# Kernel tuning notes

Measured on AMD Instinct MI355X. Metric: run time of the kernel, lower is better.

Reference implementation:

```python
import jax, jax.numpy as jnp
import numpy as np

B, S, E = 2, 2048, 2048
H, D = 16, 128
I = 8192
EPS = 1e-5


def layernorm(x, w, b):
    mu = jnp.mean(x, axis=-1, keepdims=True)
    var = jnp.mean(jnp.square(x - mu), axis=-1, keepdims=True)
    return (x - mu) * jax.lax.rsqrt(var + EPS) * w + b


def setup_inputs() -> dict:
    key = jax.random.key(0)
    ks = jax.random.split(key, 6)
    s = 0.02
    return {
        "x": jax.random.normal(ks[0], (B, S, E), jnp.float32),
        "ln1_w": jnp.ones((E,), jnp.float32),
        "ln1_b": jnp.zeros((E,), jnp.float32),
        "Wqkv": jax.random.normal(ks[1], (E, 3 * E), jnp.float32) * s,
        "Wo": jax.random.normal(ks[2], (E, E), jnp.float32) * s,
        "ln2_w": jnp.ones((E,), jnp.float32),
        "ln2_b": jnp.zeros((E,), jnp.float32),
        "W1": jax.random.normal(ks[3], (E, I), jnp.float32) * s,
        "W2": jax.random.normal(ks[4], (I, E), jnp.float32) * s,
    }


def reference(x, ln1_w, ln1_b, Wqkv, Wo, ln2_w, ln2_b, W1, W2):
    scale = D ** -0.5
    # --- attention sublayer (pre-LN) ---
    h = layernorm(x, ln1_w, ln1_b)
    qkv = (h @ Wqkv).reshape(B, S, 3, H, D)
    q, k, v = [jnp.moveaxis(qkv[:, :, i], 1, 2) for i in range(3)]  # [B,H,S,D]
    scores = jnp.einsum("bhqd,bhkd->bhqk", q, k) * scale
    causal = jnp.triu(jnp.ones((S, S), bool), k=1)
    scores = jnp.where(causal, -jnp.inf, scores)
    attn = jax.nn.softmax(scores, axis=-1)
    out = jnp.einsum("bhqk,bhkd->bqhd", attn, v).reshape(B, S, E)
    x = x + out @ Wo
    # --- FFN sublayer (pre-LN) ---
    h = layernorm(x, ln2_w, ln2_b)
    x = x + jax.nn.gelu(h @ W1, approximate=True) @ W2
    return x
```

## Files before the change

kernel.cpp:

```cpp
#include <hip/hip_runtime.h>
#include <hip/hip_bf16.h>

#define B_ 2
#define S_ 2048
#define E_ 2048
#define H_ 16
#define D_ 128
#define I_ 8192
#define T_ (B_*S_)

typedef __attribute__((ext_vector_type(8))) short bf16x8;
typedef __attribute__((ext_vector_type(8))) unsigned short us8;
typedef __attribute__((ext_vector_type(4))) float f32x4;

__device__ __forceinline__ unsigned short f2bf(float f) {
  union { float f; unsigned int u; } c; c.f = f;
  unsigned int u = c.u;
  unsigned int r = (u + 0x7fffu + ((u >> 16) & 1u)) >> 16;
  return (unsigned short)r;
}

__device__ __forceinline__ void gload16(const void* g, void* l) {
  __builtin_amdgcn_global_load_lds((const __attribute__((address_space(1))) void*)g,
                                   (__attribute__((address_space(3))) void*)l, 16, 0, 0);
}

__global__ void transpose_w(const float* __restrict__ in, unsigned short* __restrict__ out,
                            int K, int N) {
  __shared__ float tile[32][33];
  const int n0 = blockIdx.x * 32, k0 = blockIdx.y * 32;
  const int tx = threadIdx.x, ty = threadIdx.y;
#pragma unroll
  for (int j = 0; j < 4; ++j) {
    int k = k0 + ty + j * 8;
    tile[ty + j * 8][tx] = in[(size_t)k * N + n0 + tx];
  }
  __syncthreads();
#pragma unroll
  for (int j = 0; j < 4; ++j) {
    int n = n0 + ty + j * 8;
    out[(size_t)n * K + k0 + tx] = f2bf(tile[tx][ty + j * 8]);
  }
}

__global__ void ln_kernel(const float* __restrict__ x, const float* __restrict__ w,
                          const float* __restrict__ b, unsigned short* __restrict__ out) {
  const int row = blockIdx.x;
  const int tid = threadIdx.x;
  const int wid = tid >> 6, lane = tid & 63;
  const float4* xr = (const float4*)(x + (size_t)row * E_);
  float4 v0 = xr[tid * 2], v1 = xr[tid * 2 + 1];
  float s  = v0.x + v0.y + v0.z + v0.w + v1.x + v1.y + v1.z + v1.w;
  float sq = v0.x*v0.x + v0.y*v0.y + v0.z*v0.z + v0.w*v0.w
           + v1.x*v1.x + v1.y*v1.y + v1.z*v1.z + v1.w*v1.w;
#pragma unroll
  for (int off = 32; off > 0; off >>= 1) {
    s  += __shfl_xor(s, off);
    sq += __shfl_xor(sq, off);
  }
  __shared__ float red[8];
  if (lane == 0) { red[wid] = s; red[wid + 4] = sq; }
  __syncthreads();
  s  = red[0] + red[1] + red[2] + red[3];
  sq = red[4] + red[5] + red[6] + red[7];
  const float mu  = s * (1.0f / E_);
  const float var = sq * (1.0f / E_) - mu * mu;
  const float rstd = rsqrtf(var + 1e-5f);
  const float4* w4 = (const float4*)w + tid * 2;
  const float4* b4 = (const float4*)b + tid * 2;
  float4 w0 = w4[0], w1 = w4[1], bb0 = b4[0], bb1 = b4[1];
  us8 o;
  o[0] = f2bf((v0.x - mu) * rstd * w0.x + bb0.x);
  o[1] = f2bf((v0.y - mu) * rstd * w0.y + bb0.y);
  o[2] = f2bf((v0.z - mu) * rstd * w0.z + bb0.z);
  o[3] = f2bf((v0.w - mu) * rstd * w0.w + bb0.w);
  o[4] = f2bf((v1.x - mu) * rstd * w1.x + bb1.x);
  o[5] = f2bf((v1.y - mu) * rstd * w1.y + bb1.y);
  o[6] = f2bf((v1.z - mu) * rstd * w1.z + bb1.z);
  o[7] = f2bf((v1.w - mu) * rstd * w1.w + bb1.w);
  *(us8*)(&out[(size_t)row * E_ + tid * 8]) = o;
}

template<int EPI>
__global__ void gemm_bt(const unsigned short* __restrict__ A,
                        const unsigned short* __restrict__ Bt,
                        void* __restrict__ Cout,
                        const float* __restrict__ resid,
                        int M, int N, int K) {
  __shared__ __align__(16) unsigned short As[128 * 32];
  __shared__ __align__(16) unsigned short Bs[128 * 32];
  const int gn = N >> 7;
  const int nwg = (M >> 7) * gn;
  const int cpx = nwg >> 3;
  const int bid = blockIdx.x;
  const int swz = (bid & 7) * cpx + (bid >> 3);
  const int bm = swz / gn, bn = swz % gn;
  const int tid = threadIdx.x;
  const int wid = tid >> 6, lane = tid & 63;
  const int fr = lane & 15, kg = lane >> 4;
  const int wr = wid >> 1, wc = wid & 1;

  const int c0 = wid * 2;
  const unsigned short* gA = A  + (size_t)(bm * 128 + c0 * 16 + (lane >> 2)) * K + (lane & 3) * 8;
  const unsigned short* gB = Bt + (size_t)(bn * 128 + c0 * 16 + (lane >> 2)) * K + (lane & 3) * 8;
  unsigned short* lA = &As[c0 * 512];
  unsigned short* lB = &Bs[c0 * 512];

  const unsigned short* rA = &As[(wr * 64 + fr) * 32 + kg * 8];
  const unsigned short* rB = &Bs[(wc * 64 + fr) * 32 + kg * 8];

  f32x4 acc[4][4] = {};
  const int nk = K >> 5;
  for (int kt = 0; kt < nk; ++kt) {
    __syncthreads();
    gload16(gA,                 lA);
    gload16(gA + 16 * (size_t)K, lA + 512);
    gload16(gB,                 lB);
    gload16(gB + 16 * (size_t)K, lB + 512);
    gA += 32; gB += 32;
    __syncthreads();
    bf16x8 af[4], bfr[4];
#pragma unroll
    for (int m = 0; m < 4; ++m) af[m]  = *(const bf16x8*)(rA + m * 16 * 32);
#pragma unroll
    for (int n = 0; n < 4; ++n) bfr[n] = *(const bf16x8*)(rB + n * 16 * 32);
#pragma unroll
    for (int m = 0; m < 4; ++m)
#pragma unroll
      for (int n = 0; n < 4; ++n)
        acc[m][n] = __builtin_amdgcn_mfma_f32_16x16x32_bf16(af[m], bfr[n], acc[m][n], 0, 0, 0);
  }

  const int row0 = bm * 128 + wr * 64;
  const int col0 = bn * 128 + wc * 64;
#pragma unroll
  for (int m = 0; m < 4; ++m) {
#pragma unroll
    for (int n = 0; n < 4; ++n) {
#pragma unroll
      for (int r = 0; r < 4; ++r) {
        const int row = row0 + m * 16 + kg * 4 + r;
        const int col = col0 + n * 16 + fr;
        const size_t idx = (size_t)row * N + col;
        const float v = acc[m][n][r];
        if constexpr (EPI == 0) {
          ((unsigned short*)Cout)[idx] = f2bf(v);
        } else if constexpr (EPI == 1) {
          const float u = 0.7978845608028654f * (v + 0.044715f * v * v * v);
          const float gel = 0.5f * v * (1.0f + tanhf(u));
          ((unsigned short*)Cout)[idx] = f2bf(gel);
        } else {
          ((float*)Cout)[idx] = v + resid[idx];
        }
      }
    }
  }
}

__global__ void extract_vT(const unsigned short* __restrict__ qkv, unsigned short* __restrict__ vT) {
  __shared__ unsigned short tile[32][34];
  const int bh = blockIdx.z;
  const int b = bh >> 4, h = bh & 15;
  const int s0 = blockIdx.y * 32, d0 = blockIdx.x * 32;
  const int tx = threadIdx.x, ty = threadIdx.y;
#pragma unroll
  for (int j = 0; j < 4; ++j) {
    int s = s0 + ty + j * 8;
    tile[ty + j * 8][tx] = qkv[(size_t)(b * S_ + s) * 6144 + 4096 + h * 128 + d0 + tx];
  }
  __syncthreads();
#pragma unroll
  for (int j = 0; j < 4; ++j) {
    int d = d0 + ty + j * 8;
    vT[((size_t)bh * 128 + d) * 2048 + s0 + tx] = tile[tx][ty + j * 8];
  }
}

__global__ void attn_kernel(const unsigned short* __restrict__ qkv,
                            const unsigned short* __restrict__ vT,
                            unsigned short* __restrict__ outp) {
  __shared__ __align__(16) unsigned short Ks[64 * 136];
  __shared__ __align__(16) unsigned short Vts[128 * 72];
  __shared__ __align__(16) unsigned short Ps[4 * 16 * 40];
  const int qt = blockIdx.x;
  const int bh = blockIdx.y;
  const int b = bh >> 4, h = bh & 15;
  const int tid = threadIdx.x, wid = tid >> 6, lane = tid & 63;
  const int fr = lane & 15, g = lane >> 4;

  const unsigned short* qptr = qkv + (size_t)(b * S_ + qt * 64 + wid * 16 + fr) * 6144 + h * 128;
  bf16x8 qf[4];
#pragma unroll
  for (int dc = 0; dc < 4; ++dc) qf[dc] = *(const bf16x8*)(qptr + dc * 32 + g * 8);

  float m0[4], l0[4];
#pragma unroll
  for (int r = 0; r < 4; ++r) { m0[r] = -1e30f; l0[r] = 0.0f; }
  f32x4 acc[8] = {};

  const unsigned short* kbase = qkv + (size_t)(b * S_) * 6144 + 2048 + h * 128;
  const unsigned short* vbase = vT + (size_t)bh * 128 * 2048;
  unsigned short* Pw = &Ps[wid * 640];
  const float scale = 0.08838834764831845f;

  for (int kt = 0; kt <= qt; ++kt) {
#pragma unroll
    for (int j = 0; j < 4; ++j) {
      int cc = tid + 256 * j;
      int krow = cc >> 4, cp = cc & 15;
      us8 v = *(const us8*)(kbase + (size_t)(kt * 64 + krow) * 6144 + cp * 8);
      *(us8*)(&Ks[krow * 136 + cp * 8]) = v;
    }
#pragma unroll
    for (int j = 0; j < 4; ++j) {
      int cc = tid + 256 * j;
      int drow = cc >> 3, cp = cc & 7;
      us8 v = *(const us8*)(vbase + (size_t)drow * 2048 + kt * 64 + cp * 8);
      *(us8*)(&Vts[drow * 72 + cp * 8]) = v;
    }
    __syncthreads();
    const bool diag = (kt == qt);
    for (int half = 0; half < 2; ++half) {
      f32x4 sc[2] = {};
#pragma unroll
      for (int dc = 0; dc < 4; ++dc) {
#pragma unroll
        for (int sub = 0; sub < 2; ++sub) {
          bf16x8 kf = *(const bf16x8*)(&Ks[(half * 32 + sub * 16 + fr) * 136 + dc * 32 + g * 8]);
          sc[sub] = __builtin_amdgcn_mfma_f32_16x16x32_bf16(qf[dc], kf, sc[sub], 0, 0, 0);
        }
      }
      float p[2][4];
#pragma unroll
      for (int sub = 0; sub < 2; ++sub)
#pragma unroll
        for (int r = 0; r < 4; ++r) {
          float v = sc[sub][r] * scale;
          if (diag) {
            int key = kt * 64 + half * 32 + sub * 16 + fr;
            int qr  = qt * 64 + wid * 16 + g * 4 + r;
            if (key > qr) v = -1e30f;
          }
          p[sub][r] = v;
        }
      float corr[4];
#pragma unroll
      for (int r = 0; r < 4; ++r) {
        float mx = fmaxf(p[0][r], p[1][r]);
#pragma unroll
        for (int off = 1; off < 16; off <<= 1) mx = fmaxf(mx, __shfl_xor(mx, off));
        const float mn = fmaxf(m0[r], mx);
        corr[r] = __expf(m0[r] - mn);
        m0[r] = mn;
        p[0][r] = __expf(p[0][r] - mn);
        p[1][r] = __expf(p[1][r] - mn);
        float rs = p[0][r] + p[1][r];
#pragma unroll
        for (int off = 1; off < 16; off <<= 1) rs += __shfl_xor(rs, off);
        l0[r] = l0[r] * corr[r] + rs;
      }
#pragma unroll
      for (int dt = 0; dt < 8; ++dt)
#pragma unroll
        for (int r = 0; r < 4; ++r) acc[dt][r] *= corr[r];
#pragma unroll
      for (int sub = 0; sub < 2; ++sub)
#pragma unroll
        for (int r = 0; r < 4; ++r)
          Pw[(g * 4 + r) * 40 + sub * 16 + fr] = f2bf(p[sub][r]);
      bf16x8 pf = *(const bf16x8*)(&Pw[fr * 40 + g * 8]);
#pragma unroll
      for (int dt = 0; dt < 8; ++dt) {
        bf16x8 vf = *(const bf16x8*)(&Vts[(dt * 16 + fr) * 72 + half * 32 + g * 8]);
        acc[dt] = __builtin_amdgcn_mfma_f32_16x16x32_bf16(pf, vf, acc[dt], 0, 0, 0);
      }
    }
    __syncthreads();
  }
  float inv[4];
#pragma unroll
  for (int r = 0; r < 4; ++r) inv[r] = 1.0f / l0[r];
#pragma unroll
  for (int dt = 0; dt < 8; ++dt)
#pragma unroll
    for (int r = 0; r < 4; ++r) {
      const size_t row = (size_t)(b * S_ + qt * 64 + wid * 16 + g * 4 + r);
      outp[row * E_ + h * 128 + dt * 16 + fr] = f2bf(acc[dt][r] * inv[r]);
    }
}

extern "C" void kernel_launch(void* const* d_in, const int* in_sizes, int n_in,
                              void* d_out, int out_size, void* d_ws, size_t ws_size,
                              hipStream_t stream) {
  (void)in_sizes; (void)n_in; (void)out_size; (void)ws_size;
  const float* x    = (const float*)d_in[0];
  const float* ln1w = (const float*)d_in[1];
  const float* ln1b = (const float*)d_in[2];
  const float* Wqkv = (const float*)d_in[3];
  const float* Wo   = (const float*)d_in[4];
  const float* ln2w = (const float*)d_in[5];
  const float* ln2b = (const float*)d_in[6];
  const float* W1   = (const float*)d_in[7];
  const float* W2   = (const float*)d_in[8];
  float* out = (float*)d_out;
  char* ws = (char*)d_ws;

  unsigned short* WqkvT = (unsigned short*)(ws + 0);
  unsigned short* WoT   = (unsigned short*)(ws + 25165824);
  unsigned short* W1T   = (unsigned short*)(ws + 33554432);
  unsigned short* W2T   = (unsigned short*)(ws + 67108864);
  unsigned short* qkvb  = (unsigned short*)(ws + 100663296);
  unsigned short* vTb   = (unsigned short*)(ws + 150994944);
  unsigned short* gbuf  = (unsigned short*)(ws + 100663296);
  unsigned short* hbuf  = (unsigned short*)(ws + 167772160);
  float*          x1    = (float*)         (ws + 184549376);

  const dim3 tb(32, 8);
  hipLaunchKernelGGL(transpose_w, dim3(6144 / 32, 2048 / 32), tb, 0, stream, Wqkv, WqkvT, 2048, 6144);
  hipLaunchKernelGGL(transpose_w, dim3(2048 / 32, 2048 / 32), tb, 0, stream, Wo,   WoT,   2048, 2048);
  hipLaunchKernelGGL(transpose_w, dim3(8192 / 32, 2048 / 32), tb, 0, stream, W1,   W1T,   2048, 8192);
  hipLaunchKernelGGL(transpose_w, dim3(2048 / 32, 8192 / 32), tb, 0, stream, W2,   W2T,   8192, 2048);

  hipLaunchKernelGGL(ln_kernel, dim3(T_), dim3(256), 0, stream, x, ln1w, ln1b, hbuf);
  hipLaunchKernelGGL((gemm_bt<0>), dim3(32 * 48), dim3(256), 0, stream,
                     hbuf, WqkvT, (void*)qkvb, (const float*)nullptr, T_, 6144, 2048);
  hipLaunchKernelGGL(extract_vT, dim3(4, 64, 32), tb, 0, stream, qkvb, vTb);
  hipLaunchKernelGGL(attn_kernel, dim3(S_ / 64, B_ * H_), dim3(256), 0, stream, qkvb, vTb, hbuf);
  hipLaunchKernelGGL((gemm_bt<2>), dim3(32 * 16), dim3(256), 0, stream,
                     hbuf, WoT, (void*)x1, x, T_, 2048, 2048);
  hipLaunchKernelGGL(ln_kernel, dim3(T_), dim3(256), 0, stream, x1, ln2w, ln2b, hbuf);
  hipLaunchKernelGGL((gemm_bt<1>), dim3(32 * 64), dim3(256), 0, stream,
                     hbuf, W1T, (void*)gbuf, (const float*)nullptr, T_, 8192, 2048);
  hipLaunchKernelGGL((gemm_bt<2>), dim3(32 * 16), dim3(256), 0, stream,
                     gbuf, W2T, (void*)out, x1, T_, 2048, 8192);
}
```

Before: 853.3 us.

## Prefetch K/V tiles into registers, swizzle LDS, process full 64-key tile per softmax

```diff
diff --git a/kernel.cpp b/kernel.cpp
--- a/kernel.cpp
+++ b/kernel.cpp
@@ -176,11 +176,12 @@
   }
 }
 
-__global__ void attn_kernel(const unsigned short* __restrict__ qkv,
-                            const unsigned short* __restrict__ vT,
-                            unsigned short* __restrict__ outp) {
-  __shared__ __align__(16) unsigned short Ks[64 * 136];
-  __shared__ __align__(16) unsigned short Vts[128 * 72];
+__global__ __launch_bounds__(256, 4)
+void attn_kernel(const unsigned short* __restrict__ qkv,
+                 const unsigned short* __restrict__ vT,
+                 unsigned short* __restrict__ outp) {
+  __shared__ __align__(16) unsigned short Ks[64 * 128];
+  __shared__ __align__(16) unsigned short Vts[128 * 64];
   __shared__ __align__(16) unsigned short Ps[4 * 16 * 40];
   const int qt = blockIdx.x;
   const int bh = blockIdx.y;
@@ -203,80 +204,98 @@
   unsigned short* Pw = &Ps[wid * 640];
   const float scale = 0.08838834764831845f;
 
+  us8 kreg[4], vreg[4];
+#pragma unroll
+  for (int j = 0; j < 4; ++j) {
+    const int cc = tid + 256 * j;
+    kreg[j] = *(const us8*)(kbase + (size_t)(cc >> 4) * 6144 + (cc & 15) * 8);
+    vreg[j] = *(const us8*)(vbase + (size_t)(cc >> 3) * 2048 + (cc & 7) * 8);
+  }
+
   for (int kt = 0; kt <= qt; ++kt) {
+    __syncthreads();
 #pragma unroll
     for (int j = 0; j < 4; ++j) {
-      int cc = tid + 256 * j;
-      int krow = cc >> 4, cp = cc & 15;
-      us8 v = *(const us8*)(kbase + (size_t)(kt * 64 + krow) * 6144 + cp * 8);
-      *(us8*)(&Ks[krow * 136 + cp * 8]) = v;
-    }
-#pragma unroll
-    for (int j = 0; j < 4; ++j) {
-      int cc = tid + 256 * j;
-      int drow = cc >> 3, cp = cc & 7;
-      us8 v = *(const us8*)(vbase + (size_t)drow * 2048 + kt * 64 + cp * 8);
-      *(us8*)(&Vts[drow * 72 + cp * 8]) = v;
+      const int cc = tid + 256 * j;
+      const int krow = cc >> 4, kcp = cc & 15;
+      *(us8*)(&Ks[krow * 128 + ((kcp * 8) ^ ((krow & 7) << 3))]) = kreg[j];
+      const int drow = cc >> 3, vcp = cc & 7;
+      *(us8*)(&Vts[drow * 64 + ((vcp * 8) ^ ((drow & 7) << 3))]) = vreg[j];
+    }
+    if (kt < qt) {
+#pragma unroll
+      for (int j = 0; j < 4; ++j) {
+        const int cc = tid + 256 * j;
+        kreg[j] = *(const us8*)(kbase + (size_t)((kt + 1) * 64 + (cc >> 4)) * 6144 + (cc & 15) * 8);
+        vreg[j] = *(const us8*)(vbase + (size_t)(cc >> 3) * 2048 + (kt + 1) * 64 + (cc & 7) * 8);
+      }
     }
     __syncthreads();
+
+    f32x4 sc[4] = {};
+    __builtin_amdgcn_s_setprio(1);
+#pragma unroll
+    for (int dc = 0; dc < 4; ++dc) {
+#pragma unroll
+      for (int sub = 0; sub < 4; ++sub) {
+        const int row = sub * 16 + fr;
+        bf16x8 kf = *(const bf16x8*)(&Ks[row * 128 + ((dc * 32 + g * 8) ^ ((row & 7) << 3))]);
+        sc[sub] = __builtin_amdgcn_mfma_f32_16x16x32_bf16(qf[dc], kf, sc[sub], 0, 0, 0);
+      }
+    }
+    __builtin_amdgcn_s_setprio(0);
+
+    float p[4][4];
     const bool diag = (kt == qt);
+#pragma unroll
+    for (int sub = 0; sub < 4; ++sub) {
+#pragma unroll
+      for (int r = 0; r < 4; ++r) {
+        float v = sc[sub][r] * scale;
+        if (diag && (sub * 16 + fr > wid * 16 + g * 4 + r)) v = -1e30f;
+        p[sub][r] = v;
+      }
+    }
+    float corr[4];
+#pragma unroll
+    for (int r = 0; r < 4; ++r) {
+      float mx = fmaxf(fmaxf(p[0][r], p[1][r]), fmaxf(p[2][r], p[3][r]));
+#pragma unroll
+      for (int off = 1; off < 16; off <<= 1) mx = fmaxf(mx, __shfl_xor(mx, off));
+      const float mn = fmaxf(m0[r], mx);
+      corr[r] = __expf(m0[r] - mn);
+      m0[r] = mn;
+      float rs = 0.0f;
+#pragma unroll
+      for (int sub = 0; sub < 4; ++sub) { p[sub][r] = __expf(p[sub][r] - mn); rs += p[sub][r]; }
+#pragma unroll
+      for (int off = 1; off < 16; off <<= 1) rs += __shfl_xor(rs, off);
+      l0[r] = l0[r] * corr[r] + rs;
+    }
+#pragma unroll
+    for (int dt = 0; dt < 8; ++dt)
+#pragma unroll
+      for (int r = 0; r < 4; ++r) acc[dt][r] *= corr[r];
+
+#pragma unroll
     for (int half = 0; half < 2; ++half) {
-      f32x4 sc[2] = {};
-#pragma unroll
-      for (int dc = 0; dc < 4; ++dc) {
-#pragma unroll
-        for (int sub = 0; sub < 2; ++sub) {
-          bf16x8 kf = *(const bf16x8*)(&Ks[(half * 32 + sub * 16 + fr) * 136 + dc * 32 + g * 8]);
-          sc[sub] = __builtin_amdgcn_mfma_f32_16x16x32_bf16(qf[dc], kf, sc[sub], 0, 0, 0);
-        }
-      }
-      float p[2][4];
-#pragma unroll
-      for (int sub = 0; sub < 2; ++sub)
-#pragma unroll
-        for (int r = 0; r < 4; ++r) {
-          float v = sc[sub][r] * scale;
-          if (diag) {
-            int key = kt * 64 + half * 32 + sub * 16 + fr;
-            int qr  = qt * 64 + wid * 16 + g * 4 + r;
-            if (key > qr) v = -1e30f;
-          }
-          p[sub][r] = v;
-        }
-      float corr[4];
-#pragma unroll
-      for (int r = 0; r < 4; ++r) {
-        float mx = fmaxf(p[0][r], p[1][r]);
-#pragma unroll
-        for (int off = 1; off < 16; off <<= 1) mx = fmaxf(mx, __shfl_xor(mx, off));
-        const float mn = fmaxf(m0[r], mx);
-        corr[r] = __expf(m0[r] - mn);
-        m0[r] = mn;
-        p[0][r] = __expf(p[0][r] - mn);
-        p[1][r] = __expf(p[1][r] - mn);
-        float rs = p[0][r] + p[1][r];
-#pragma unroll
-        for (int off = 1; off < 16; off <<= 1) rs += __shfl_xor(rs, off);
-        l0[r] = l0[r] * corr[r] + rs;
-      }
-#pragma unroll
-      for (int dt = 0; dt < 8; ++dt)
-#pragma unroll
-        for (int r = 0; r < 4; ++r) acc[dt][r] *= corr[r];
-#pragma unroll
-      for (int sub = 0; sub < 2; ++sub)
+#pragma unroll
+      for (int s2 = 0; s2 < 2; ++s2)
 #pragma unroll
         for (int r = 0; r < 4; ++r)
-          Pw[(g * 4 + r) * 40 + sub * 16 + fr] = f2bf(p[sub][r]);
+          Pw[(g * 4 + r) * 40 + s2 * 16 + fr] = f2bf(p[half * 2 + s2][r]);
       bf16x8 pf = *(const bf16x8*)(&Pw[fr * 40 + g * 8]);
+      __builtin_amdgcn_s_setprio(1);
 #pragma unroll
       for (int dt = 0; dt < 8; ++dt) {
-        bf16x8 vf = *(const bf16x8*)(&Vts[(dt * 16 + fr) * 72 + half * 32 + g * 8]);
+        const int row = dt * 16 + fr;
+        bf16x8 vf = *(const bf16x8*)(&Vts[row * 64 + ((half * 32 + g * 8) ^ ((row & 7) << 3))]);
         acc[dt] = __builtin_amdgcn_mfma_f32_16x16x32_bf16(pf, vf, acc[dt], 0, 0, 0);
       }
-    }
-    __syncthreads();
-  }
+      __builtin_amdgcn_s_setprio(0);
+    }
+  }
+
   float inv[4];
 #pragma unroll
   for (int r = 0; r < 4; ++r) inv[r] = 1.0f / l0[r];
```

Result: slower. 909.7 us (+6.6%).
